# Performance work log

Measured on AMD Instinct MI355X. Metric: run time of the kernel, lower is better.

Reference implementation:

```python
import jax, jax.numpy as jnp
import numpy as np
import math

B, S, E = 2, 2048, 2048
H = 16
DH = E // H            # 128
L = 64                 # latent_dim
EB = 128               # effective block size (== block_size, adjuster init = log(block_size))
KB = 4 * EB            # kv block size = 512


def setup_inputs() -> dict:
    key = jax.random.key(0)
    ks = jax.random.split(key, 16)
    s_e = 1.0 / math.sqrt(E)
    s_dh = 1.0 / math.sqrt(DH)
    return {
        "x": jax.random.normal(ks[0], (B, S, E), jnp.float32),
        "Wq": jax.random.normal(ks[1], (E, E), jnp.float32) * s_e,
        "bq": jnp.zeros((E,), jnp.float32),
        "Wk": jax.random.normal(ks[2], (E, E), jnp.float32) * s_e,
        "bk": jnp.zeros((E,), jnp.float32),
        "Wv": jax.random.normal(ks[3], (E, E), jnp.float32) * s_e,
        "bv": jnp.zeros((E,), jnp.float32),
        "Wo": jax.random.normal(ks[4], (E, E), jnp.float32) * s_e,
        "bo": jnp.zeros((E,), jnp.float32),
        "Wql": jax.random.normal(ks[5], (DH, L), jnp.float32) * s_dh,
        "bql": jnp.zeros((L,), jnp.float32),
        "Wkl": jax.random.normal(ks[6], (DH, L), jnp.float32) * s_dh,
        "bkl": jnp.zeros((L,), jnp.float32),
        "Wm": jax.random.normal(ks[7], (DH, DH), jnp.float32) * s_dh,
        "bm": jnp.zeros((DH,), jnp.float32),
    }


def _split_heads(t):
    # [B,S,E] -> [B,H,S,DH]
    return t.reshape(B, S, H, DH).transpose(0, 2, 1, 3)


def reference(x, Wq, bq, Wk, bk, Wv, bv, Wo, bo, Wql, bql, Wkl, bkl, Wm, bm):
    q = _split_heads(x @ Wq + bq)
    k = _split_heads(x @ Wk + bk)
    v = _split_heads(x @ Wv + bv)

    # elu+1 feature maps on latent projections
    q_lat = jax.nn.elu(q @ Wql + bql) + 1.0  # [B,H,S,L]
    k_lat = jax.nn.elu(k @ Wkl + bkl) + 1.0  # [B,H,S,L]

    nq, nk = S // EB, S // KB
    qb = q_lat.reshape(B, H, nq, EB, L)
    kb = k_lat.reshape(B, H, nk, KB, L)
    vb = v.reshape(B, H, nk, KB, DH)

    scale = 1.0 / math.sqrt(L)
    # per-(q block, kv block) scores: [B,H,nq,nk,EB,KB]
    scores = jnp.einsum("bhqel,bhkfl->bhqkef", qb, kb) * scale
    # softmax independently over each kv block (axis = f), then SUM over kv blocks
    probs = jax.nn.softmax(scores, axis=-1)
    out = jnp.einsum("bhqkef,bhkfd->bhqed", probs, vb)  # [B,H,nq,EB,DH]
    out = out.reshape(B, H, S, DH)

    # latent mixer: Linear(head_dim) -> gelu
    mixed = jax.nn.gelu(out @ Wm + bm)

    y = mixed.transpose(0, 2, 1, 3).reshape(B, S, E)
    return y @ Wo + bo
```

## Files before the change

kernel.cpp:

```cpp
#include <hip/hip_runtime.h>
#include <stdint.h>
#include <math.h>

#define B_ 2
#define S_ 2048
#define E_ 2048
#define H_ 16
#define DH_ 128
#define L_ 64

typedef unsigned short u16;
typedef __attribute__((ext_vector_type(4))) float f32x4;
typedef __attribute__((ext_vector_type(8))) short short8;
typedef __attribute__((ext_vector_type(4))) short short4v;

__device__ __forceinline__ u16 f2bf(float f) {
    union { float f; uint32_t u; } c; c.f = f;
    uint32_t u = c.u + 0x7fff + ((c.u >> 16) & 1);
    return (u16)(u >> 16);
}
__device__ __forceinline__ u16 f2bf_ru(float f) {
    union { float f; uint32_t u; } c; c.f = f;
    return (u16)((c.u + 0x8000u) >> 16);
}
__device__ __forceinline__ float bf2f(u16 h) {
    union { uint32_t u; float f; } c; c.u = ((uint32_t)h) << 16;
    return c.f;
}
__device__ __forceinline__ float elu1(float x) {
    return x > 0.f ? x + 1.f : __expf(x);
}
__device__ __forceinline__ float gelu_tanh(float x) {
    float z = 0.7978845608028654f * (x + 0.044715f * x * x * x);
    float az = fabsf(z);
    float e = __expf(-2.f * az);
    float t = (1.f - e) / (1.f + e);
    t = (z >= 0.f) ? t : -t;
    return 0.5f * x * (1.f + t);
}
__device__ __forceinline__ void async16(u16* lds_dst, const u16* g_src) {
    __builtin_amdgcn_global_load_lds(
        (const __attribute__((address_space(1))) uint32_t*)g_src,
        (__attribute__((address_space(3))) uint32_t*)lds_dst, 16, 0, 0);
}
__device__ __forceinline__ int swz_off(int row, int chunk) {
    return ((chunk ^ (row & 7)) << 3);
}

__global__ __launch_bounds__(256) void cvt_bf16(const float* __restrict__ in,
                                                u16* __restrict__ out, int n8) {
    for (int i = blockIdx.x * 256 + threadIdx.x; i < n8; i += gridDim.x * 256) {
        float4 a = reinterpret_cast<const float4*>(in)[2 * i];
        float4 b = reinterpret_cast<const float4*>(in)[2 * i + 1];
        u16 u[8] __attribute__((aligned(16)));
        u[0] = f2bf(a.x); u[1] = f2bf(a.y); u[2] = f2bf(a.z); u[3] = f2bf(a.w);
        u[4] = f2bf(b.x); u[5] = f2bf(b.y); u[6] = f2bf(b.z); u[7] = f2bf(b.w);
        reinterpret_cast<int4*>(out)[i] = *(const int4*)u;
    }
}

__global__ __launch_bounds__(256) void wtrans(const float* __restrict__ W,
                                              u16* __restrict__ Wt, int K, int N) {
    __shared__ u16 t[64][68];
    const int tid = threadIdx.x;
    const int n0 = blockIdx.x * 64, k0 = blockIdx.y * 64;
    const int c4 = (tid & 15) * 4, r = tid >> 4;
    #pragma unroll
    for (int i = 0; i < 4; i++) {
        int row = r + 16 * i;
        float4 v = *reinterpret_cast<const float4*>(&W[(size_t)(k0 + row) * N + n0 + c4]);
        t[c4 + 0][row] = f2bf(v.x); t[c4 + 1][row] = f2bf(v.y);
        t[c4 + 2][row] = f2bf(v.z); t[c4 + 3][row] = f2bf(v.w);
    }
    __syncthreads();
    #pragma unroll
    for (int i = 0; i < 4; i++) {
        int nr = r + 16 * i;
        ushort4 o = *reinterpret_cast<const ushort4*>(&t[nr][c4]);
        *reinterpret_cast<ushort4*>(&Wt[(size_t)(n0 + nr) * K + k0 + c4]) = o;
    }
}

__global__ __launch_bounds__(256) void beff_kernel(
    const float* __restrict__ b, const float* __restrict__ Wl,
    const float* __restrict__ bl, float* __restrict__ beff, int outoff)
{
    int t = blockIdx.x * 256 + threadIdx.x;
    if (t >= 1024) return;
    int h = t >> 6, n = t & 63;
    float s = bl[n];
    for (int d = 0; d < 128; d++) s += b[h * 128 + d] * Wl[d * 64 + n];
    beff[outoff + t] = s;
}

__global__ __launch_bounds__(256) void bveff_kernel(
    const float* __restrict__ bv, const float* __restrict__ Wm,
    float* __restrict__ bveff)
{
    int t = blockIdx.x * 256 + threadIdx.x;
    if (t >= 2048) return;
    int h = t >> 7, n = t & 127;
    float s = 0.f;
    for (int d = 0; d < 128; d++) s += bv[h * 128 + d] * Wm[d * 128 + n];
    bveff[t] = s;
}

__global__ __launch_bounds__(256) void weff_kernel(
    const float* __restrict__ W, const u16* __restrict__ Wlt,
    u16* __restrict__ Wefft, int outoff)
{
    __shared__ u16 lds[8192 + 16384];
    const int tid = threadIdx.x, l = tid & 63, w = tid >> 6;
    const int k0 = blockIdx.x * 128, h = blockIdx.y;

    #pragma unroll
    for (int i = 0; i < 4; i++) {
        int lin = i * 256 + tid, row = lin >> 4, c = lin & 15;
        async16(&lds[lin * 8], &Wlt[row * 128 + swz_off(row, c)]);
    }
    #pragma unroll
    for (int i = 0; i < 16; i++) {
        int e = (i * 256 + tid) * 4;
        int row = e >> 7, ec = e & 127;
        float4 v4 = *reinterpret_cast<const float4*>(
            &W[(size_t)(k0 + row) * E_ + h * DH_ + ec]);
        u16 u[4] __attribute__((aligned(8)));
        u[0] = f2bf(v4.x); u[1] = f2bf(v4.y); u[2] = f2bf(v4.z); u[3] = f2bf(v4.w);
        int chunk = ec >> 3, half = (ec >> 2) & 1;
        *reinterpret_cast<uint64_t*>(
            &lds[8192 + row * 128 + swz_off(row, chunk) + half * 4]) = *(const uint64_t*)u;
    }
    __syncthreads();

    f32x4 zero = {0.f, 0.f, 0.f, 0.f};
    f32x4 acc[8];
    #pragma unroll
    for (int nt = 0; nt < 8; nt++) acc[nt] = zero;
    #pragma unroll
    for (int ks = 0; ks < 4; ks++) {
        int arow = 16 * w + (l & 15);
        short8 af = *reinterpret_cast<const short8*>(
            &lds[arow * 128 + swz_off(arow, ks * 4 + (l >> 4))]);
        #pragma unroll
        for (int nt = 0; nt < 8; nt++) {
            int brow = 16 * nt + (l & 15);
            short8 bf = *reinterpret_cast<const short8*>(
                &lds[8192 + brow * 128 + swz_off(brow, ks * 4 + (l >> 4))]);
            acc[nt] = __builtin_amdgcn_mfma_f32_16x16x32_bf16(af, bf, acc[nt], 0, 0, 0);
        }
    }
    #pragma unroll
    for (int nt = 0; nt < 8; nt++) {
        int kc = k0 + 16 * nt + (l & 15);
        #pragma unroll
        for (int j = 0; j < 4; j++) {
            int nl = 16 * w + (l >> 4) * 4 + j;
            Wefft[(size_t)(outoff + h * 64 + nl) * E_ + kc] = f2bf(acc[nt][j]);
        }
    }
}

__global__ __launch_bounds__(256) void weffv_kernel(
    const float* __restrict__ Wv, const u16* __restrict__ Wmt,
    u16* __restrict__ Wv2t)
{
    __shared__ u16 lds[16384 + 16384];
    const int tid = threadIdx.x, l = tid & 63, w = tid >> 6;
    const int e0 = blockIdx.x * 128, h = blockIdx.y;

    #pragma unroll
    for (int i = 0; i < 8; i++) {
        int lin = i * 256 + tid, row = lin >> 4, c = lin & 15;
        async16(&lds[lin * 8], &Wmt[row * 128 + swz_off(row, c)]);
    }
    #pragma unroll
    for (int i = 0; i < 16; i++) {
        int e = (i * 256 + tid) * 4;
        int row = e >> 7, ec = e & 127;
        float4 v4 = *reinterpret_cast<const float4*>(
            &Wv[(size_t)(e0 + row) * E_ + h * DH_ + ec]);
        u16 u[4] __attribute__((aligned(8)));
        u[0] = f2bf(v4.x); u[1] = f2bf(v4.y); u[2] = f2bf(v4.z); u[3] = f2bf(v4.w);
        int chunk = ec >> 3, half = (ec >> 2) & 1;
        *reinterpret_cast<uint64_t*>(
            &lds[16384 + row * 128 + swz_off(row, chunk) + half * 4]) = *(const uint64_t*)u;
    }
    __syncthreads();

    f32x4 zero = {0.f, 0.f, 0.f, 0.f};
    f32x4 acc[2][8];
    #pragma unroll
    for (int mi = 0; mi < 2; mi++)
        #pragma unroll
        for (int nt = 0; nt < 8; nt++) acc[mi][nt] = zero;
    #pragma unroll
    for (int ks = 0; ks < 4; ks++) {
        short8 af[2];
        #pragma unroll
        for (int mi = 0; mi < 2; mi++) {
            int arow = 32 * w + 16 * mi + (l & 15);
            af[mi] = *reinterpret_cast<const short8*>(
                &lds[arow * 128 + swz_off(arow, ks * 4 + (l >> 4))]);
        }
        #pragma unroll
        for (int nt = 0; nt < 8; nt++) {
            int brow = 16 * nt + (l & 15);
            short8 bf = *reinterpret_cast<const short8*>(
                &lds[16384 + brow * 128 + swz_off(brow, ks * 4 + (l >> 4))]);
            #pragma unroll
            for (int mi = 0; mi < 2; mi++)
                acc[mi][nt] = __builtin_amdgcn_mfma_f32_16x16x32_bf16(af[mi], bf, acc[mi][nt], 0, 0, 0);
        }
    }
    #pragma unroll
    for (int mi = 0; mi < 2; mi++)
        #pragma unroll
        for (int nt = 0; nt < 8; nt++) {
            int ec = e0 + 16 * nt + (l & 15);
            #pragma unroll
            for (int j = 0; j < 4; j++) {
                int dp = 32 * w + 16 * mi + (l >> 4) * 4 + j;
                Wv2t[(size_t)(h * 128 + dp) * E_ + ec] = f2bf(acc[mi][nt][j]);
            }
        }
}

template <typename OutT, bool DUAL, int EPI>
__global__ __launch_bounds__(256) void gemm_bf16(
    const u16* __restrict__ A, const u16* __restrict__ A2,
    const u16* __restrict__ Wt, const float* __restrict__ bias,
    OutT* __restrict__ C, u16* __restrict__ latq, u16* __restrict__ latk,
    int M, int N, int K)
{
    __shared__ u16 lds[DUAL ? 24576 : 16384];
    const int tid = threadIdx.x, l = tid & 63, w = tid >> 6;
    const int wr = w >> 1, wc = w & 1;
    const int row0 = blockIdx.y * 128, col0 = blockIdx.x * 128;

    f32x4 zero = {0.f, 0.f, 0.f, 0.f};
    f32x4 acc[4][4];
    #pragma unroll
    for (int i = 0; i < 4; i++)
        #pragma unroll
        for (int j = 0; j < 4; j++) acc[i][j] = zero;

    for (int k0 = 0; k0 < K; k0 += 64) {
        #pragma unroll
        for (int i = 0; i < 4; i++) {
            int lin = i * 256 + tid, row = lin >> 3, c = lin & 7;
            int sc = swz_off(row, c);
            async16(&lds[lin * 8], &A[(size_t)(row0 + row) * K + k0 + sc]);
            async16(&lds[8192 + lin * 8], &Wt[(size_t)(col0 + row) * K + k0 + sc]);
            if (DUAL) async16(&lds[16384 + lin * 8], &A2[(size_t)(row0 + row) * K + k0 + sc]);
        }
        __syncthreads();
        #pragma unroll
        for (int ks = 0; ks < 2; ks++) {
            short8 af[4], bf[4], af2[4];
            #pragma unroll
            for (int mi = 0; mi < 4; mi++) {
                int row = 64 * wr + 16 * mi + (l & 15);
                int idx = row * 64 + swz_off(row, ks * 4 + (l >> 4));
                af[mi] = *reinterpret_cast<const short8*>(&lds[idx]);
                if (DUAL) af2[mi] = *reinterpret_cast<const short8*>(&lds[16384 + idx]);
            }
            #pragma unroll
            for (int ni = 0; ni < 4; ni++) {
                int row = 64 * wc + 16 * ni + (l & 15);
                int idx = 8192 + row * 64 + swz_off(row, ks * 4 + (l >> 4));
                bf[ni] = *reinterpret_cast<const short8*>(&lds[idx]);
            }
            #pragma unroll
            for (int mi = 0; mi < 4; mi++)
                #pragma unroll
                for (int ni = 0; ni < 4; ni++) {
                    acc[mi][ni] = __builtin_amdgcn_mfma_f32_16x16x32_bf16(
                        af[mi], bf[ni], acc[mi][ni], 0, 0, 0);
                    if (DUAL)
                        acc[mi][ni] = __builtin_amdgcn_mfma_f32_16x16x32_bf16(
                            af2[mi], bf[ni], acc[mi][ni], 0, 0, 0);
                }
        }
        __syncthreads();
    }
    #pragma unroll
    for (int mi = 0; mi < 4; mi++)
        #pragma unroll
        for (int ni = 0; ni < 4; ni++) {
            int col = col0 + 64 * wc + 16 * ni + (l & 15);
            float bv = (EPI == 2) ? 0.f : bias[col];
            #pragma unroll
            for (int j = 0; j < 4; j++) {
                int row = row0 + 64 * wr + 16 * mi + (l >> 4) * 4 + j;
                float v = acc[mi][ni][j] + ((EPI == 2) ? bias[row] : bv);
                if (EPI == 1) {
                    v = elu1(v);
                    if (col < 1024) v *= 0.125f;
                    u16* dst = (col < 1024) ? latq : latk;
                    int h = (col >> 6) & 15, n = col & 63;
                    int bb = row >> 11, s = row & 2047;
                    dst[(((size_t)bb * 16 + h) * S_ + s) * 64 + n] = f2bf(v);
                } else if (EPI == 2) {
                    int d = row & 127, hh = row >> 7;
                    int bb = col >> 11, s = col & 2047;
                    ((u16*)C)[((size_t)((bb << 4) + hh) * 128 + d) * (size_t)S_ + s] = f2bf(v);
                } else if (sizeof(OutT) == 2) {
                    C[(size_t)row * N + col] = (OutT)f2bf(v);
                } else {
                    C[(size_t)row * N + col] = (OutT)v;
                }
            }
        }
}

__global__ __launch_bounds__(256, 2) void attn_mfma(
    const u16* __restrict__ qlat, const u16* __restrict__ klat,
    const u16* __restrict__ Vt, const float* __restrict__ bm,
    u16* __restrict__ mixed)
{
    __shared__ u16 pool[32768];
    const int tid = threadIdx.x, l = tid & 63, w = tid >> 6;
    const int g = l >> 4;
    const int qi = blockIdx.x, bh = blockIdx.y;
    const int bb = bh >> 4, h = bh & 15;
    const u16* klat_bh = klat + (size_t)bh * S_ * L_;
    const u16* vt_bh = Vt + (size_t)bh * 128 * S_;
    const int q0 = qi * 128;

    #pragma unroll
    for (int i = 0; i < 4; i++) {
        int lin = i * 256 + tid, row = lin >> 3, c = lin & 7;
        async16(&pool[lin * 8],
                &qlat[((size_t)bh * S_ + q0 + row) * 64 + swz_off(row, c)]);
    }
    #pragma unroll
    for (int i = 0; i < 2; i++) {
        int lin = i * 256 + tid, row = lin >> 3, c = lin & 7;
        async16(&pool[8192 + lin * 8], &klat_bh[(size_t)row * 64 + swz_off(row, c)]);
    }
    #pragma unroll
    for (int i = 0; i < 4; i++) {
        int lin = i * 256 + tid, d = lin >> 3, c = lin & 7;
        async16(&pool[16384 + lin * 8], &vt_bh[(size_t)d * S_ + swz_off(d, c)]);
    }
    __syncthreads();

    short8 qf[2][2];
    #pragma unroll
    for (int qt = 0; qt < 2; qt++)
        #pragma unroll
        for (int ks = 0; ks < 2; ks++) {
            int row = 32 * w + 16 * qt + (l & 15);
            qf[qt][ks] = *reinterpret_cast<const short8*>(
                &pool[row * 64 + swz_off(row, ks * 4 + g)]);
        }

    f32x4 zero = {0.f, 0.f, 0.f, 0.f};
    f32x4 Ot[8][2], Op[8][2];
    float l_reg[2];
    #pragma unroll
    for (int nd = 0; nd < 8; nd++)
        #pragma unroll
        for (int qt = 0; qt < 2; qt++) { Ot[nd][qt] = zero; Op[nd][qt] = zero; }
    #pragma unroll
    for (int qt = 0; qt < 2; qt++) l_reg[qt] = 0.f;

    for (int t = 0; t < 32; t++) {
        const int cur = t & 1;
        if (t < 31) {
            const int f0 = (t + 1) * 64, nb = cur ^ 1;
            #pragma unroll
            for (int i = 0; i < 2; i++) {
                int lin = i * 256 + tid, row = lin >> 3, c = lin & 7;
                async16(&pool[8192 + nb * 4096 + lin * 8],
                        &klat_bh[(size_t)(f0 + row) * 64 + swz_off(row, c)]);
            }
            #pragma unroll
            for (int i = 0; i < 4; i++) {
                int lin = i * 256 + tid, d = lin >> 3, c = lin & 7;
                async16(&pool[16384 + nb * 8192 + lin * 8],
                        &vt_bh[(size_t)d * S_ + f0 + swz_off(d, c)]);
            }
        }
        const u16* Kb = &pool[8192 + cur * 4096];
        const u16* Vb = &pool[16384 + cur * 8192];

        f32x4 accS[4][2];
        #pragma unroll
        for (int fi = 0; fi < 4; fi++)
            #pragma unroll
            for (int qt = 0; qt < 2; qt++) accS[fi][qt] = zero;
        #pragma unroll
        for (int ks = 0; ks < 2; ks++) {
            short8 kfrag[4];
            #pragma unroll
            for (int fi = 0; fi < 4; fi++) {
                int row = 16 * fi + (l & 15);
                kfrag[fi] = *reinterpret_cast<const short8*>(
                    &Kb[row * 64 + swz_off(row, ks * 4 + g)]);
            }
            #pragma unroll
            for (int fi = 0; fi < 4; fi++)
                #pragma unroll
                for (int qt = 0; qt < 2; qt++)
                    accS[fi][qt] = __builtin_amdgcn_mfma_f32_16x16x32_bf16(
                        kfrag[fi], qf[qt][ks], accS[fi][qt], 0, 0, 0);
        }

        short4v pf[2][4];
        #pragma unroll
        for (int qt = 0; qt < 2; qt++) {
            float sum = 0.f;
            #pragma unroll
            for (int fi = 0; fi < 4; fi++) {
                float p[4];
                #pragma unroll
                for (int j = 0; j < 4; j++) {
                    p[j] = __expf(accS[fi][qt][j]);
                    sum += p[j];
                }
                short4v pk;
                pk[0] = (short)f2bf_ru(p[0]); pk[1] = (short)f2bf_ru(p[1]);
                pk[2] = (short)f2bf_ru(p[2]); pk[3] = (short)f2bf_ru(p[3]);
                pf[qt][fi] = pk;
            }
            sum += __shfl_xor(sum, 16);
            sum += __shfl_xor(sum, 32);
            l_reg[qt] += sum;
        }

        #pragma unroll
        for (int kt = 0; kt < 4; kt++) {
            int fl = 16 * kt + 4 * g;
            int fch = fl >> 3, fsub = fl & 7;
            #pragma unroll
            for (int nd = 0; nd < 8; nd++) {
                int d = 16 * nd + (l & 15);
                short4v vfrag = *reinterpret_cast<const short4v*>(
                    &Vb[d * 64 + ((fch ^ (d & 7)) << 3) + fsub]);
                #pragma unroll
                for (int qt = 0; qt < 2; qt++)
                    Op[nd][qt] = __builtin_amdgcn_mfma_f32_16x16x16bf16_1k(
                        vfrag, pf[qt][kt], Op[nd][qt], 0, 0, 0);
            }
        }

        if ((t & 7) == 7) {
            #pragma unroll
            for (int qt = 0; qt < 2; qt++) {
                float linv = 1.f / l_reg[qt];
                #pragma unroll
                for (int nd = 0; nd < 8; nd++) {
                    Ot[nd][qt] += Op[nd][qt] * linv;
                    Op[nd][qt] = zero;
                }
                l_reg[qt] = 0.f;
            }
        }
        __syncthreads();
    }

    #pragma unroll
    for (int nd = 0; nd < 8; nd++)
        #pragma unroll
        for (int qt = 0; qt < 2; qt++) {
            int q = q0 + 32 * w + 16 * qt + (l & 15);
            u16 hi4[4] __attribute__((aligned(8)));
            #pragma unroll
            for (int j = 0; j < 4; j++) {
                int d = 16 * nd + 4 * g + j;
                float v = gelu_tanh(Ot[nd][qt][j] + bm[d]);
                hi4[j] = f2bf(v);
            }
            size_t o = ((size_t)(bb * S_ + q)) * E_ + h * DH_ + 16 * nd + 4 * g;
            *reinterpret_cast<ushort4*>(&mixed[o]) = *(const ushort4*)hi4;
        }
}

extern "C" void kernel_launch(void* const* d_in, const int* in_sizes, int n_in,
                              void* d_out, int out_size, void* d_ws, size_t ws_size,
                              hipStream_t stream)
{
    const float* x   = (const float*)d_in[0];
    const float* Wq  = (const float*)d_in[1];
    const float* bq  = (const float*)d_in[2];
    const float* Wk  = (const float*)d_in[3];
    const float* bk  = (const float*)d_in[4];
    const float* Wv  = (const float*)d_in[5];
    const float* bv  = (const float*)d_in[6];
    const float* Wo  = (const float*)d_in[7];
    const float* bo  = (const float*)d_in[8];
    const float* Wql = (const float*)d_in[9];
    const float* bql = (const float*)d_in[10];
    const float* Wkl = (const float*)d_in[11];
    const float* bkl = (const float*)d_in[12];
    const float* Wm  = (const float*)d_in[13];
    const float* bm  = (const float*)d_in[14];
    float* out = (float*)d_out;

    u16* ws0   = (u16*)d_ws;
    u16* xb    = ws0;
    u16* Wefft = ws0 + 8388608;
    u16* Wv2t  = Wefft + 4194304;
    u16* Wot   = Wv2t + 4194304;
    u16* Wmt   = Wot + 4194304;
    u16* Wqlt  = Wmt + 16384;
    u16* Wklt  = Wqlt + 8192;
    float* beff  = (float*)(Wklt + 8192);
    float* bveff = beff + 2048;
    u16* Vt    = (u16*)(bveff + 2048);
    u16* qlat  = Vt + 8388608;
    u16* klat  = qlat + 4194304;
    u16* mixed = xb;

    dim3 gemm_g(16, 32);
    dim3 gemmv_g(32, 16);
    dim3 attn_g(16, 32);

    cvt_bf16<<<2048, 256, 0, stream>>>(x, xb, 1048576);
    wtrans<<<dim3(32, 32), 256, 0, stream>>>(Wo, Wot, 2048, 2048);
    wtrans<<<dim3(2, 2), 256, 0, stream>>>(Wm, Wmt, 128, 128);
    wtrans<<<dim3(1, 2), 256, 0, stream>>>(Wql, Wqlt, 128, 64);
    wtrans<<<dim3(1, 2), 256, 0, stream>>>(Wkl, Wklt, 128, 64);
    beff_kernel<<<4, 256, 0, stream>>>(bq, Wql, bql, beff, 0);
    beff_kernel<<<4, 256, 0, stream>>>(bk, Wkl, bkl, beff, 1024);
    bveff_kernel<<<8, 256, 0, stream>>>(bv, Wm, bveff);
    weff_kernel<<<dim3(16, 16), 256, 0, stream>>>(Wq, Wqlt, Wefft, 0);
    weff_kernel<<<dim3(16, 16), 256, 0, stream>>>(Wk, Wklt, Wefft, 1024);
    weffv_kernel<<<dim3(16, 16), 256, 0, stream>>>(Wv, Wmt, Wv2t);

    gemm_bf16<u16, false, 1><<<gemm_g, 256, 0, stream>>>(
        xb, nullptr, Wefft, beff, (u16*)nullptr, qlat, klat, 4096, 2048, 2048);
    gemm_bf16<u16, false, 2><<<gemmv_g, 256, 0, stream>>>(
        Wv2t, nullptr, xb, bveff, Vt, nullptr, nullptr, 2048, 4096, 2048);
    attn_mfma<<<attn_g, 256, 0, stream>>>(qlat, klat, Vt, bm, mixed);
    gemm_bf16<float, false, 0><<<gemm_g, 256, 0, stream>>>(
        mixed, nullptr, Wot, bo, out, nullptr, nullptr, 4096, 2048, 2048);
}
```

Baseline: 268.1 us.

## Merge prep kernels and fuse Q/K latent and V projections into one GEMM

Combines the small weight transpose and bias-fold kernels into one small_prep launch, and the three effective-weight kernels into one weff3 launch. The V projection is now computed as extra output columns (2048..4095) of the same GEMM that produces the Q/K latents, with the epilogue writing V transposed per head. This removes several launches and the separate V GEMM, and gives one larger 32x32-tile grid in place of two. In exchange the V output is written with a column-indexed transposed store pattern and the epilogue carries more branching.

```diff
diff --git a/kernel.cpp b/kernel.cpp
--- a/kernel.cpp
+++ b/kernel.cpp
@@ -59,59 +59,74 @@
     }
 }
 
-__global__ __launch_bounds__(256) void wtrans(const float* __restrict__ W,
-                                              u16* __restrict__ Wt, int K, int N) {
-    __shared__ u16 t[64][68];
+__device__ void wtrans_body(u16* sp, const float* __restrict__ W,
+                            u16* __restrict__ Wt, int K, int N, int bx, int by) {
     const int tid = threadIdx.x;
-    const int n0 = blockIdx.x * 64, k0 = blockIdx.y * 64;
+    const int n0 = bx * 64, k0 = by * 64;
     const int c4 = (tid & 15) * 4, r = tid >> 4;
     #pragma unroll
     for (int i = 0; i < 4; i++) {
         int row = r + 16 * i;
         float4 v = *reinterpret_cast<const float4*>(&W[(size_t)(k0 + row) * N + n0 + c4]);
-        t[c4 + 0][row] = f2bf(v.x); t[c4 + 1][row] = f2bf(v.y);
-        t[c4 + 2][row] = f2bf(v.z); t[c4 + 3][row] = f2bf(v.w);
+        sp[(c4 + 0) * 68 + row] = f2bf(v.x); sp[(c4 + 1) * 68 + row] = f2bf(v.y);
+        sp[(c4 + 2) * 68 + row] = f2bf(v.z); sp[(c4 + 3) * 68 + row] = f2bf(v.w);
     }
     __syncthreads();
     #pragma unroll
     for (int i = 0; i < 4; i++) {
         int nr = r + 16 * i;
-        ushort4 o = *reinterpret_cast<const ushort4*>(&t[nr][c4]);
+        ushort4 o = *reinterpret_cast<const ushort4*>(&sp[nr * 68 + c4]);
         *reinterpret_cast<ushort4*>(&Wt[(size_t)(n0 + nr) * K + k0 + c4]) = o;
     }
 }
 
-__global__ __launch_bounds__(256) void beff_kernel(
-    const float* __restrict__ b, const float* __restrict__ Wl,
-    const float* __restrict__ bl, float* __restrict__ beff, int outoff)
-{
-    int t = blockIdx.x * 256 + threadIdx.x;
-    if (t >= 1024) return;
-    int h = t >> 6, n = t & 63;
-    float s = bl[n];
-    for (int d = 0; d < 128; d++) s += b[h * 128 + d] * Wl[d * 64 + n];
-    beff[outoff + t] = s;
-}
-
-__global__ __launch_bounds__(256) void bveff_kernel(
-    const float* __restrict__ bv, const float* __restrict__ Wm,
-    float* __restrict__ bveff)
-{
-    int t = blockIdx.x * 256 + threadIdx.x;
-    if (t >= 2048) return;
-    int h = t >> 7, n = t & 127;
-    float s = 0.f;
-    for (int d = 0; d < 128; d++) s += bv[h * 128 + d] * Wm[d * 128 + n];
-    bveff[t] = s;
-}
-
-__global__ __launch_bounds__(256) void weff_kernel(
-    const float* __restrict__ W, const u16* __restrict__ Wlt,
-    u16* __restrict__ Wefft, int outoff)
-{
-    __shared__ u16 lds[8192 + 16384];
+__global__ __launch_bounds__(256) void wtrans(const float* __restrict__ W,
+                                              u16* __restrict__ Wt, int K, int N) {
+    __shared__ u16 sp[64 * 68];
+    wtrans_body(sp, W, Wt, K, N, blockIdx.x, blockIdx.y);
+}
+
+__global__ __launch_bounds__(256) void small_prep(
+    const float* __restrict__ Wm, const float* __restrict__ Wql,
+    const float* __restrict__ Wkl, const float* __restrict__ bq,
+    const float* __restrict__ bk, const float* __restrict__ bv,
+    const float* __restrict__ bql, const float* __restrict__ bkl,
+    u16* __restrict__ Wmt, u16* __restrict__ Wqlt, u16* __restrict__ Wklt,
+    float* __restrict__ beff)
+{
+    __shared__ u16 sp[64 * 68];
+    const int blk = blockIdx.x, tid = threadIdx.x;
+    if (blk < 4) {
+        wtrans_body(sp, Wm, Wmt, 128, 128, blk & 1, blk >> 1);
+    } else if (blk < 6) {
+        wtrans_body(sp, Wql, Wqlt, 128, 64, 0, blk - 4);
+    } else if (blk < 8) {
+        wtrans_body(sp, Wkl, Wklt, 128, 64, 0, blk - 6);
+    } else if (blk < 16) {
+        const float* b  = (blk < 12) ? bq : bk;
+        const float* Wl = (blk < 12) ? Wql : Wkl;
+        const float* bl = (blk < 12) ? bql : bkl;
+        int outoff = (blk < 12) ? 0 : 1024;
+        int t = ((blk - 8) & 3) * 256 + tid;
+        int h = t >> 6, n = t & 63;
+        float s = bl[n];
+        for (int d = 0; d < 128; d++) s += b[h * 128 + d] * Wl[d * 64 + n];
+        beff[outoff + t] = s;
+    } else {
+        int t = (blk - 16) * 256 + tid;
+        int h = t >> 7, n = t & 127;
+        float s = 0.f;
+        for (int d = 0; d < 128; d++) s += bv[h * 128 + d] * Wm[d * 128 + n];
+        beff[2048 + t] = s;
+    }
+}
+
+__device__ void weff_body(u16* lds, const float* __restrict__ W,
+                          const u16* __restrict__ Wlt, u16* __restrict__ Wefft,
+                          int outoff, int kblk, int h)
+{
     const int tid = threadIdx.x, l = tid & 63, w = tid >> 6;
-    const int k0 = blockIdx.x * 128, h = blockIdx.y;
+    const int k0 = kblk * 128;
 
     #pragma unroll
     for (int i = 0; i < 4; i++) {
@@ -160,13 +175,12 @@
     }
 }
 
-__global__ __launch_bounds__(256) void weffv_kernel(
-    const float* __restrict__ Wv, const u16* __restrict__ Wmt,
-    u16* __restrict__ Wv2t)
-{
-    __shared__ u16 lds[16384 + 16384];
+__device__ void weffv_body(u16* lds, const float* __restrict__ Wv,
+                           const u16* __restrict__ Wmt, u16* __restrict__ Wv2t,
+                           int eblk, int h)
+{
     const int tid = threadIdx.x, l = tid & 63, w = tid >> 6;
-    const int e0 = blockIdx.x * 128, h = blockIdx.y;
+    const int e0 = eblk * 128;
 
     #pragma unroll
     for (int i = 0; i < 8; i++) {
@@ -225,14 +239,31 @@
         }
 }
 
-template <typename OutT, bool DUAL, int EPI>
+__global__ __launch_bounds__(256) void weff3(
+    const float* __restrict__ Wq, const float* __restrict__ Wk,
+    const float* __restrict__ Wv, const u16* __restrict__ Wqlt,
+    const u16* __restrict__ Wklt, const u16* __restrict__ Wmt,
+    u16* __restrict__ Wefft)
+{
+    __shared__ u16 lds[32768];
+    const int blk = blockIdx.x;
+    if (blk < 256) {
+        weff_body(lds, Wq, Wqlt, Wefft, 0, blk & 15, blk >> 4);
+    } else if (blk < 512) {
+        weff_body(lds, Wk, Wklt, Wefft, 1024, (blk - 256) & 15, (blk - 256) >> 4);
+    } else {
+        weffv_body(lds, Wv, Wmt, Wefft + (size_t)2048 * E_, (blk - 512) & 15, (blk - 512) >> 4);
+    }
+}
+
+template <typename OutT, int EPI>
 __global__ __launch_bounds__(256) void gemm_bf16(
-    const u16* __restrict__ A, const u16* __restrict__ A2,
-    const u16* __restrict__ Wt, const float* __restrict__ bias,
-    OutT* __restrict__ C, u16* __restrict__ latq, u16* __restrict__ latk,
+    const u16* __restrict__ A, const u16* __restrict__ Wt,
+    const float* __restrict__ bias, OutT* __restrict__ C,
+    u16* __restrict__ latq, u16* __restrict__ latk, u16* __restrict__ latv,
     int M, int N, int K)
 {
-    __shared__ u16 lds[DUAL ? 24576 : 16384];
+    __shared__ u16 lds[16384];
     const int tid = threadIdx.x, l = tid & 63, w = tid >> 6;
     const int wr = w >> 1, wc = w & 1;
     const int row0 = blockIdx.y * 128, col0 = blockIdx.x * 128;
@@ -251,35 +282,29 @@
             int sc = swz_off(row, c);
             async16(&lds[lin * 8], &A[(size_t)(row0 + row) * K + k0 + sc]);
             async16(&lds[8192 + lin * 8], &Wt[(size_t)(col0 + row) * K + k0 + sc]);
-            if (DUAL) async16(&lds[16384 + lin * 8], &A2[(size_t)(row0 + row) * K + k0 + sc]);
         }
         __syncthreads();
         #pragma unroll
         for (int ks = 0; ks < 2; ks++) {
-            short8 af[4], bf[4], af2[4];
+            short8 af[4], bf[4];
             #pragma unroll
             for (int mi = 0; mi < 4; mi++) {
                 int row = 64 * wr + 16 * mi + (l & 15);
-                int idx = row * 64 + swz_off(row, ks * 4 + (l >> 4));
-                af[mi] = *reinterpret_cast<const short8*>(&lds[idx]);
-                if (DUAL) af2[mi] = *reinterpret_cast<const short8*>(&lds[16384 + idx]);
+                af[mi] = *reinterpret_cast<const short8*>(
+                    &lds[row * 64 + swz_off(row, ks * 4 + (l >> 4))]);
             }
             #pragma unroll
             for (int ni = 0; ni < 4; ni++) {
                 int row = 64 * wc + 16 * ni + (l & 15);
-                int idx = 8192 + row * 64 + swz_off(row, ks * 4 + (l >> 4));
-                bf[ni] = *reinterpret_cast<const short8*>(&lds[idx]);
+                bf[ni] = *reinterpret_cast<const short8*>(
+                    &lds[8192 + row * 64 + swz_off(row, ks * 4 + (l >> 4))]);
             }
             #pragma unroll
             for (int mi = 0; mi < 4; mi++)
                 #pragma unroll
-                for (int ni = 0; ni < 4; ni++) {
+                for (int ni = 0; ni < 4; ni++)
                     acc[mi][ni] = __builtin_amdgcn_mfma_f32_16x16x32_bf16(
                         af[mi], bf[ni], acc[mi][ni], 0, 0, 0);
-                    if (DUAL)
-                        acc[mi][ni] = __builtin_amdgcn_mfma_f32_16x16x32_bf16(
-                            af2[mi], bf[ni], acc[mi][ni], 0, 0, 0);
-                }
         }
         __syncthreads();
     }
@@ -288,22 +313,24 @@
         #pragma unroll
         for (int ni = 0; ni < 4; ni++) {
             int col = col0 + 64 * wc + 16 * ni + (l & 15);
-            float bv = (EPI == 2) ? 0.f : bias[col];
+            float bv = bias[col];
             #pragma unroll
             for (int j = 0; j < 4; j++) {
                 int row = row0 + 64 * wr + 16 * mi + (l >> 4) * 4 + j;
-                float v = acc[mi][ni][j] + ((EPI == 2) ? bias[row] : bv);
+                float v = acc[mi][ni][j] + bv;
                 if (EPI == 1) {
-                    v = elu1(v);
-                    if (col < 1024) v *= 0.125f;
-                    u16* dst = (col < 1024) ? latq : latk;
-                    int h = (col >> 6) & 15, n = col & 63;
                     int bb = row >> 11, s = row & 2047;
-                    dst[(((size_t)bb * 16 + h) * S_ + s) * 64 + n] = f2bf(v);
-                } else if (EPI == 2) {
-                    int d = row & 127, hh = row >> 7;
-                    int bb = col >> 11, s = col & 2047;
-                    ((u16*)C)[((size_t)((bb << 4) + hh) * 128 + d) * (size_t)S_ + s] = f2bf(v);
+                    if (col < 2048) {
+                        v = elu1(v);
+                        if (col < 1024) v *= 0.125f;
+                        u16* dst = (col < 1024) ? latq : latk;
+                        int h = (col >> 6) & 15, n = col & 63;
+                        dst[(((size_t)bb * 16 + h) * S_ + s) * 64 + n] = f2bf(v);
+                    } else {
+                        int c2 = col - 2048;
+                        int d = c2 & 127, hh = c2 >> 7;
+                        latv[((size_t)((bb << 4) + hh) * 128 + d) * (size_t)S_ + s] = f2bf(v);
+                    }
                 } else if (sizeof(OutT) == 2) {
                     C[(size_t)row * N + col] = (OutT)f2bf(v);
                 } else {
@@ -501,39 +528,29 @@
     u16* ws0   = (u16*)d_ws;
     u16* xb    = ws0;
     u16* Wefft = ws0 + 8388608;
-    u16* Wv2t  = Wefft + 4194304;
-    u16* Wot   = Wv2t + 4194304;
+    u16* Wot   = Wefft + 8388608;
     u16* Wmt   = Wot + 4194304;
     u16* Wqlt  = Wmt + 16384;
     u16* Wklt  = Wqlt + 8192;
-    float* beff  = (float*)(Wklt + 8192);
-    float* bveff = beff + 2048;
-    u16* Vt    = (u16*)(bveff + 2048);
+    float* beff = (float*)(Wklt + 8192);
+    u16* Vt    = (u16*)(beff + 4096);
     u16* qlat  = Vt + 8388608;
     u16* klat  = qlat + 4194304;
     u16* mixed = xb;
 
+    dim3 proj_g(32, 32);
     dim3 gemm_g(16, 32);
-    dim3 gemmv_g(32, 16);
     dim3 attn_g(16, 32);
 
     cvt_bf16<<<2048, 256, 0, stream>>>(x, xb, 1048576);
     wtrans<<<dim3(32, 32), 256, 0, stream>>>(Wo, Wot, 2048, 2048);
-    wtrans<<<dim3(2, 2), 256, 0, stream>>>(Wm, Wmt, 128, 128);
-    wtrans<<<dim3(1, 2), 256, 0, stream>>>(Wql, Wqlt, 128, 64);
-    wtrans<<<dim3(1, 2), 256, 0, stream>>>(Wkl, Wklt, 128, 64);
-    beff_kernel<<<4, 256, 0, stream>>>(bq, Wql, bql, beff, 0);
-    beff_kernel<<<4, 256, 0, stream>>>(bk, Wkl, bkl, beff, 1024);
-    bveff_kernel<<<8, 256, 0, stream>>>(bv, Wm, bveff);
-    weff_kernel<<<dim3(16, 16), 256, 0, stream>>>(Wq, Wqlt, Wefft, 0);
-    weff_kernel<<<dim3(16, 16), 256, 0, stream>>>(Wk, Wklt, Wefft, 1024);
-    weffv_kernel<<<dim3(16, 16), 256, 0, stream>>>(Wv, Wmt, Wv2t);
-
-    gemm_bf16<u16, false, 1><<<gemm_g, 256, 0, stream>>>(
-        xb, nullptr, Wefft, beff, (u16*)nullptr, qlat, klat, 4096, 2048, 2048);
-    gemm_bf16<u16, false, 2><<<gemmv_g, 256, 0, stream>>>(
-        Wv2t, nullptr, xb, bveff, Vt, nullptr, nullptr, 2048, 4096, 2048);
+    small_prep<<<24, 256, 0, stream>>>(Wm, Wql, Wkl, bq, bk, bv, bql, bkl,
+                                       Wmt, Wqlt, Wklt, beff);
+    weff3<<<768, 256, 0, stream>>>(Wq, Wk, Wv, Wqlt, Wklt, Wmt, Wefft);
+
+    gemm_bf16<u16, 1><<<proj_g, 256, 0, stream>>>(
+        xb, Wefft, beff, (u16*)nullptr, qlat, klat, Vt, 4096, 4096, 2048);
     attn_mfma<<<attn_g, 256, 0, stream>>>(qlat, klat, Vt, bm, mixed);
-    gemm_bf16<float, false, 0><<<gemm_g, 256, 0, stream>>>(
-        mixed, nullptr, Wot, bo, out, nullptr, nullptr, 4096, 2048, 2048);
-}
+    gemm_bf16<float, 0><<<gemm_g, 256, 0, stream>>>(
+        mixed, Wot, bo, out, nullptr, nullptr, nullptr, 4096, 2048, 2048);
+}
```

Result: slower. 277.9 us (+3.7%).
